# Performance work log

Measured on AMD Instinct MI355X. Metric: run time of the kernel, lower is better.

Reference implementation:

```python
import itertools
import jax, jax.numpy as jnp
import numpy as np

# ---- static config (matches init_kwargs) ----
FRAME_H, FRAME_W = 480, 640
RES = 5               # map_resolution (cm/cell)
Z_RES = 5
MAP_SIZE_CM = 4800 // 2   # after global_downscaling
VR = 100              # vision_range
HFOV = 79.0
DU = 1                # du_scale
CAT_THR, EXP_THR, MAP_THR = 5.0, 1.0, 1.0
NSEM = 16
MAX_H = int(360 / Z_RES)    # 72
MIN_H = int(-80 / Z_RES)    # -16
AGENT_H_CM = 0.88 * 100.0
XC = (FRAME_W - 1.0) / 2.0
ZC = (FRAME_H - 1.0) / 2.0
FOCAL = (FRAME_W / 2.0) / np.tan(np.deg2rad(HFOV / 2.0))
VFOV = np.arctan(FRAME_H / 2.0 / FOCAL)
MIN_VISION = AGENT_H_CM / np.tan(VFOV)
SHIFT_X = VR * RES // 2     # shift_loc[0]; rotation angle is 0 -> identity
DEG = 57.29577951308232


def splat_feat_nd(grid_dims, feat, coords):
    # feat: (B,F,N); coords: (B,3,N) in [-1,1]; trilinear scatter-add splat.
    B, Fc, N = feat.shape
    pos_dim, wts_dim = [], []
    for d in range(3):
        g = grid_dims[d]
        pos = coords[:, d, :] * (g / 2.0) + g / 2.0
        pd, wd = [], []
        for ix in (0, 1):
            p = jnp.floor(pos) + ix
            safe = ((p > 0) & (p < g)).astype(feat.dtype)
            wd.append((1.0 - jnp.abs(pos - p)) * safe)
            pd.append(p * safe)
        pos_dim.append(pd)
        wts_dim.append(wd)
    gflat = jnp.zeros((B, Fc, grid_dims[0] * grid_dims[1] * grid_dims[2]), feat.dtype)
    scatter = jax.vmap(lambda g, i, u: g.at[:, i].add(u))
    for ix_d in itertools.product((0, 1), (0, 1), (0, 1)):
        index = jnp.zeros((B, N), feat.dtype)
        wts = jnp.ones((B, N), feat.dtype)
        for d in range(3):
            index = index * grid_dims[d] + pos_dim[d][ix_d[d]]
            wts = wts * wts_dim[d][ix_d[d]]
        upd = feat * wts[:, None, :]
        gflat = jnp.round(scatter(gflat, index.astype(jnp.int32), upd))  # torch rounds after each pass
    return gflat.reshape(B, Fc, grid_dims[0], grid_dims[1], grid_dims[2])


def affine_grid(theta, H, W):
    # torch F.affine_grid, align_corners=False (default)
    xs = (2.0 * jnp.arange(W) + 1.0) / W - 1.0
    ys = (2.0 * jnp.arange(H) + 1.0) / H - 1.0
    X, Y = jnp.meshgrid(xs, ys, indexing='xy')          # (H,W)
    base = jnp.stack([X, Y, jnp.ones_like(X)], -1)      # (H,W,3)
    return jnp.einsum('bij,hwj->bhwi', theta, base)     # (B,H,W,2)


def grid_sample(img, grid):
    # bilinear, zeros padding, align_corners=True (as in forward)
    B, C, H, W = img.shape
    x = (grid[..., 0] + 1.0) * 0.5 * (W - 1)
    y = (grid[..., 1] + 1.0) * 0.5 * (H - 1)
    x0 = jnp.floor(x)
    y0 = jnp.floor(y)

    def gather(ix, iy):
        valid = ((ix >= 0) & (ix <= W - 1) & (iy >= 0) & (iy <= H - 1)).astype(img.dtype)
        ic = jnp.clip(ix, 0, W - 1).astype(jnp.int32)
        jc = jnp.clip(iy, 0, H - 1).astype(jnp.int32)
        v = jax.vmap(lambda im, jj, ii: im[:, jj, ii])(img, jc, ic)  # (B,C,Ho,Wo)
        return v * valid[:, None]

    wx1 = x - x0
    wx0 = 1.0 - wx1
    wy1 = y - y0
    wy0 = 1.0 - wy1
    return (gather(x0, y0) * (wx0 * wy0)[:, None]
            + gather(x0 + 1, y0) * (wx1 * wy0)[:, None]
            + gather(x0, y0 + 1) * (wx0 * wy1)[:, None]
            + gather(x0 + 1, y0 + 1) * (wx1 * wy1)[:, None])


def reference(obs, pose_obs, maps_last, poses_last, agent_heights):
    bs, c, h, w = obs.shape
    depth = obs[:, 3]
    # ---- point cloud from depth (camera frame) ----
    Y = depth[:, ::DU, ::DU]
    gx = jnp.arange(w, dtype=obs.dtype)[::DU]            # pixel x (width)
    gz = jnp.arange(h - 1, -1, -1, dtype=obs.dtype)[::DU]  # flipped pixel z (height)
    X = (gx[None, None, :] - XC) * Y / FOCAL
    Z = (gz[None, :, None] - ZC) * Y / FOCAL
    Z = Z + agent_heights * 100.0   # camera elevation 0 -> rotation is identity
    X = X + SHIFT_X                 # shift_loc angle pi/2 -> rotation is identity
    # ---- normalize to [-1,1] voxel coords ----
    Xc = ((X / RES) - VR // 2.0) / VR * 2.0
    Yc = ((Y / RES) - VR // 2.0) / VR * 2.0
    Zc = ((Z / Z_RES) - (MAX_H + MIN_H) // 2.0) / (MAX_H - MIN_H) * 2.0
    coords = jnp.stack([Xc, Yc, Zc], axis=1).reshape(bs, 3, -1)   # (B,3,N)
    # ---- per-point features: [occupancy=1, avg-pooled semantics] ----
    hs, ws = h // DU, w // DU
    sem = obs[:, 4:].reshape(bs, c - 4, hs, DU, ws, DU).mean(axis=(3, 5))
    feat = jnp.concatenate([jnp.ones((bs, 1, hs * ws), obs.dtype),
                            sem.reshape(bs, c - 4, hs * ws)], axis=1)
    # ---- splat into voxel grid, then height-axis projections ----
    voxels = splat_feat_nd((VR, VR, MAX_H - MIN_H), feat, coords).swapaxes(2, 3)
    min_z = int(35 / Z_RES - MIN_H)               # 23
    max_z = int((AGENT_H_CM + 1) / Z_RES - MIN_H)  # 33
    floor_z = int(-35 / Z_RES - MIN_H)             # 9
    agent_height_proj = voxels[..., min_z:max_z].sum(-1)
    all_height_proj = voxels.sum(-1)
    mv_std = int(MIN_VISION // Z_RES)
    around_floor = voxels[..., :min_z].sum(-1)
    under_floor = (voxels[..., floor_z:min_z].sum(-1) == 0.0).astype(obs.dtype) * around_floor
    # near-field floor heuristic from last depth row
    depth_row = depth[:, -1, :]
    re_depth = jnp.where(depth_row < 3000.0, depth_row, jnp.asarray(MIN_VISION, obs.dtype))
    count = (re_depth - MIN_VISION - 60.0 > 0).sum(axis=1)
    mask = count > (w / 4.0)
    c1, c2 = (VR - 6) // 2, (VR + 6) // 2
    patch = under_floor[:, 0, mv_std, c1:c2]
    under_floor = under_floor.at[:, 0, mv_std, c1:c2].set(jnp.where(mask[:, None], 1.0, patch))
    fp_map_pred = jnp.clip((agent_height_proj[:, 0:1] + under_floor[:, 0:1]) / MAP_THR, 0.0, 1.0)
    fp_exp_pred = jnp.clip(all_height_proj[:, 0:1] / EXP_THR, 0.0, 1.0)
    # ---- paste into egocentric local map frame ----
    M = MAP_SIZE_CM // RES   # 480
    x1 = M // 2 - VR // 2
    x2 = x1 + VR
    y1 = M // 2
    y2 = y1 + VR
    agent_view = jnp.zeros((bs, c, M, M), obs.dtype)
    agent_view = agent_view.at[:, 0:1, y1:y2, x1:x2].set(fp_map_pred)
    agent_view = agent_view.at[:, 1:2, y1:y2, x1:x2].set(fp_exp_pred)
    agent_view = agent_view.at[:, 4:, y1:y2, x1:x2].set(
        jnp.clip(agent_height_proj[:, 1:] / CAT_THR, 0.0, 1.0))
    # ---- dead-reckoning pose update ----
    th = poses_last[:, 2] / DEG
    ny = poses_last[:, 1] + pose_obs[:, 0] * jnp.sin(th) + pose_obs[:, 1] * jnp.cos(th)
    nx = poses_last[:, 0] + pose_obs[:, 0] * jnp.cos(th) - pose_obs[:, 1] * jnp.sin(th)
    nt = poses_last[:, 2] + pose_obs[:, 2] * DEG
    nt = jnp.fmod(nt - 180.0, 360.0) + 180.0
    nt = jnp.fmod(nt + 180.0, 360.0) - 180.0
    current_poses = jnp.stack([nx, ny, nt], axis=1)
    # ---- spatial transform (rotate then translate) into allocentric map ----
    half = M // 2
    stx = -(nx * 100.0 / RES - half) / half
    sty = -(ny * 100.0 / RES - half) / half
    t = (90.0 - nt) * np.pi / 180.0
    cos_t, sin_t = jnp.cos(t), jnp.sin(t)
    zeros, ones = jnp.zeros_like(cos_t), jnp.ones_like(cos_t)
    theta1 = jnp.stack([jnp.stack([cos_t, -sin_t, zeros], 1),
                        jnp.stack([sin_t, cos_t, zeros], 1)], 1)
    theta2 = jnp.stack([jnp.stack([ones, zeros, stx], 1),
                        jnp.stack([zeros, ones, sty], 1)], 1)
    rotated = grid_sample(agent_view, affine_grid(theta1, M, M))
    translated = grid_sample(rotated, affine_grid(theta2, M, M))
    map_pred = jnp.maximum(maps_last, translated)
    # pose_pred aliases the in-place-updated poses_last in torch == current_poses
    return fp_map_pred, map_pred, current_poses, current_poses


def setup_inputs():
    key = jax.random.key(0)
    k1, k2, k3, k4, k5, k6 = jax.random.split(key, 6)
    bs, c, h, w = 8, 4 + NSEM, FRAME_H, FRAME_W
    obs = jax.random.uniform(k1, (bs, c, h, w), jnp.float32)            # RGB/sem in [0,1]
    depth = jax.random.uniform(k2, (bs, h, w), jnp.float32) * 480.0 + 20.0  # cm
    obs = obs.at[:, 3].set(depth)
    pose_obs = jax.random.normal(k3, (bs, 3), jnp.float32) * jnp.array([0.1, 0.1, 0.05], jnp.float32)
    maps_last = jax.random.uniform(k4, (bs, c, 480, 480), jnp.float32)
    xy = jax.random.uniform(k5, (bs, 2), jnp.float32) * 4.0 + 10.0      # meters, near map center
    ang = jax.random.uniform(k6, (bs, 1), jnp.float32) * 360.0 - 180.0
    poses_last = jnp.concatenate([xy, ang], axis=1)
    agent_heights = jnp.full((bs, 1, 1), 0.88, jnp.float32)
    return {"obs": obs, "pose_obs": pose_obs, "maps_last": maps_last,
            "poses_last": poses_last, "agent_heights": agent_heights}
```

## Files before the change

### kernel.cpp

```cpp
#include <hip/hip_runtime.h>
#include <math.h>

#pragma clang fp contract(off)

#define BS 8
#define CCH 20
#define IMH 480
#define IMW 640
#define HW (IMH*IMW)
#define VRX 100
#define NZ 88
#define NSEMC 16
#define CROP0 124
#define CROPN 232
#define NROTC 18
#define NBINS 880000
#define NBINS2 80000
#define SEMCAP 650000u

__global__ void posemask_kernel(const float* __restrict__ pose_obs,
                                const float* __restrict__ poses_last,
                                const float* __restrict__ obs,
                                float* __restrict__ outp1, float* __restrict__ outp2,
                                float* __restrict__ posebuf, float MINVF) {
#pragma clang fp contract(off)
  int b = blockIdx.x;
  int t = threadIdx.x;
  if (t == 0) {
    const float DEGF = (float)57.29577951308232;
    float th = poses_last[b*3+2] / DEGF;
    float sn = sinf(th), cs = cosf(th);
    float ny = poses_last[b*3+1] + pose_obs[b*3+0]*sn + pose_obs[b*3+1]*cs;
    float nx = poses_last[b*3+0] + pose_obs[b*3+0]*cs - pose_obs[b*3+1]*sn;
    float nt = poses_last[b*3+2] + pose_obs[b*3+2]*DEGF;
    nt = fmodf(nt - 180.0f, 360.0f) + 180.0f;
    nt = fmodf(nt + 180.0f, 360.0f) - 180.0f;
    outp1[b*3+0] = nx; outp1[b*3+1] = ny; outp1[b*3+2] = nt;
    outp2[b*3+0] = nx; outp2[b*3+1] = ny; outp2[b*3+2] = nt;
    float tt = (90.0f - nt) * (float)M_PI / 180.0f;
    float* pb = posebuf + b*8;
    pb[0] = cosf(tt);
    pb[1] = sinf(tt);
    pb[2] = -((nx*100.0f/5.0f - 240.0f)/240.0f);
    pb[3] = -((ny*100.0f/5.0f - 240.0f)/240.0f);
  }
  const float* row = obs + (size_t)b*CCH*HW + 3*(size_t)HW + 479*IMW;
  int cnt = 0;
  for (int col = t; col < IMW; col += 256) {
    float d = row[col];
    float re = (d < 3000.0f) ? d : MINVF;
    float v = re - MINVF;
    v = v - 60.0f;
    if (v > 0.0f) cnt++;
  }
  __shared__ int sh[256];
  sh[t] = cnt;
  __syncthreads();
  for (int s = 128; s > 0; s >>= 1) {
    if (t < s) sh[t] += sh[t + s];
    __syncthreads();
  }
  if (t == 0) posebuf[b*8+4] = (sh[0] > 160) ? 1.0f : 0.0f;
}

__device__ __forceinline__ void transform_pix(int r, int col, float Yd, float ah100,
                                              float FOCALF,
                                              float& pos0, float& pos1, float& pos2) {
#pragma clang fp contract(off)
  float X = ((float)col - 319.5f) * Yd / FOCALF;
  X = X + 250.0f;
  float Z = ((float)(479 - r) - 239.5f) * Yd / FOCALF;
  Z = Z + ah100;
  float Xc = (X/5.0f - 50.0f)/100.0f*2.0f;
  float Yc = (Yd/5.0f - 50.0f)/100.0f*2.0f;
  float Zc = (Z/5.0f - 28.0f)/88.0f*2.0f;
  pos0 = Xc*50.0f + 50.0f;
  pos1 = Yc*50.0f + 50.0f;
  pos2 = Zc*44.0f + 44.0f;
}

__global__ void bin_count_kernel(const float* __restrict__ obs,
                                 const float* __restrict__ agent_h,
                                 unsigned* __restrict__ cnt, unsigned* __restrict__ cnt2,
                                 float FOCALF) {
#pragma clang fp contract(off)
  int tid = blockIdx.x*256 + threadIdx.x;
#pragma unroll
  for (int u = 0; u < 4; u++) {
    int p = tid + u*614400;
    int b = p / HW;
    int pix = p - b*HW;
    int r = pix / IMW, col = pix - r*IMW;
    float Yd = obs[(size_t)b*CCH*HW + 3*(size_t)HW + pix];
    float ah100 = agent_h[b]*100.0f;
    float pos0, pos1, pos2;
    transform_pix(r, col, Yd, ah100, FOCALF, pos0, pos1, pos2);
    float f0 = floorf(pos0), f1 = floorf(pos1), f2 = floorf(pos2);
    if (f0 >= 0.0f && f0 <= 99.0f && f1 >= 0.0f && f1 <= 99.0f &&
        f2 >= 0.0f && f2 <= 87.0f) {
      int xi = (int)f0, yi = (int)f1, zi = (int)f2;
      int cb = (b*100 + yi)*100 + xi;
      atomicAdd(&cnt[cb*11 + (zi >> 3)], 1u);
      if (zi >= 22 && zi <= 32) atomicAdd(&cnt2[cb], 1u);
    }
  }
}

__device__ __forceinline__ void scan1_body(unsigned* cnt_inout,
                                           unsigned* bsum,
                                           int n, int blk, unsigned* sh) {
  int t = threadIdx.x;
  int base = blk*1024 + t*4;
  unsigned v[4];
  unsigned s = 0;
#pragma unroll
  for (int i = 0; i < 4; i++) {
    unsigned c = (base + i < n) ? cnt_inout[base + i] : 0u;
    v[i] = s; s += c;
  }
  sh[t] = s;
  __syncthreads();
  for (int off = 1; off < 256; off <<= 1) {
    unsigned add = (t >= off) ? sh[t - off] : 0u;
    __syncthreads();
    sh[t] += add;
    __syncthreads();
  }
  unsigned texcl = sh[t] - s;
#pragma unroll
  for (int i = 0; i < 4; i++)
    if (base + i < n) cnt_inout[base + i] = texcl + v[i];
  if (t == 255) bsum[blk] = sh[255];
}

__global__ void scan1m_kernel(unsigned* cnt, unsigned* bsum,
                              unsigned* cnt2, unsigned* bsum2) {
  __shared__ unsigned sh[256];
  int blk = blockIdx.x;
  if (blk < 860) scan1_body(cnt, bsum, NBINS, blk, sh);
  else           scan1_body(cnt2, bsum2, NBINS2, blk - 860, sh);
}

__global__ void scan2m_kernel(unsigned* __restrict__ bsum, unsigned* __restrict__ bsum2) {
  __shared__ unsigned sh[1024];
  unsigned* arr = (blockIdx.x == 0) ? bsum : bsum2;
  int nb = (blockIdx.x == 0) ? 860 : 79;
  int t = threadIdx.x;
  unsigned v = (t < nb) ? arr[t] : 0u;
  sh[t] = v;
  __syncthreads();
  for (int off = 1; off < 1024; off <<= 1) {
    unsigned add = (t >= off) ? sh[t - off] : 0u;
    __syncthreads();
    sh[t] += add;
    __syncthreads();
  }
  if (t < nb) arr[t] = sh[t] - v;
}

__global__ void scan3m_kernel(unsigned* __restrict__ offs, const unsigned* __restrict__ bsum,
                              unsigned* __restrict__ offs2, const unsigned* __restrict__ bsum2) {
  int blk = blockIdx.x;
  if (blk < 3438) {
    int i = blk*256 + threadIdx.x;
    if (i >= NBINS) return;
    offs[i] = offs[i] + bsum[i >> 10];
  } else {
    int i = (blk - 3438)*256 + threadIdx.x;
    if (i >= NBINS2) return;
    offs2[i] = offs2[i] + bsum2[i >> 10];
  }
}

__global__ void place_kernel(const float* __restrict__ obs,
                             const float* __restrict__ agent_h,
                             unsigned* __restrict__ offs, unsigned* __restrict__ offs2,
                             float2* __restrict__ recs,
                             float4* __restrict__ sempos, float4* __restrict__ semch,
                             float FOCALF) {
#pragma clang fp contract(off)
  int tid = blockIdx.x*256 + threadIdx.x;
#pragma unroll
  for (int u = 0; u < 2; u++) {
    int p = tid + u*1228800;
    int b = p / HW;
    int pix = p - b*HW;
    int r = pix / IMW, c = pix - r*IMW;
    const float* obsb = obs + (size_t)b*CCH*HW;
    float Yd = obsb[3*(size_t)HW + pix];
    float ah100 = agent_h[b]*100.0f;
    float pos0, pos1, pos2;
    transform_pix(r, c, Yd, ah100, FOCALF, pos0, pos1, pos2);
    float f0 = floorf(pos0), f1 = floorf(pos1), f2 = floorf(pos2);
    if (f0 >= 0.0f && f0 <= 99.0f && f1 >= 0.0f && f1 <= 99.0f &&
        f2 >= 0.0f && f2 <= 87.0f) {
      int xi = (int)f0, yi = (int)f1, zi = (int)f2;
      int cb = (b*100 + yi)*100 + xi;
      unsigned idx = atomicAdd(&offs[cb*11 + (zi >> 3)], 1u);
      recs[idx] = make_float2(__uint_as_float((unsigned)pix), Yd);
      if (zi >= 22 && zi <= 32) {
        unsigned i2 = atomicAdd(&offs2[cb], 1u);
        if (i2 < SEMCAP) {
          sempos[i2] = make_float4(pos0, pos1, pos2, 0.0f);
          float4* cp = semch + (size_t)i2*4;
#pragma unroll
          for (int q = 0; q < 4; q++) {
            cp[q] = make_float4(obsb[(size_t)(4 + q*4 + 0)*HW + pix],
                                obsb[(size_t)(4 + q*4 + 1)*HW + pix],
                                obsb[(size_t)(4 + q*4 + 2)*HW + pix],
                                obsb[(size_t)(4 + q*4 + 3)*HW + pix]);
          }
        }
      }
    }
  }
}

__global__ void __launch_bounds__(256) gatherS_cm_kernel(
    const float2* __restrict__ recs, const unsigned* __restrict__ offs,
    const float* __restrict__ agent_h, float* __restrict__ colbuf, float FOCALF) {
#pragma clang fp contract(off)
  __shared__ float S[256*9];
  __shared__ float red[32][8][4];
  int t = threadIdx.x;
  int k = t & 7, cw = t >> 3;
  int iz = k & 1, ix = (k >> 1) & 1, iy = (k >> 2) & 1;
  int col = blockIdx.x*32 + cw;
  int b = col / 10000;
  int cx = col % 100, cy = (col/100) % 100;
  float ah100 = agent_h[b]*100.0f;
  bool cellvalid = (cx+ix >= 1) && (cx+ix <= 99) && (cy+iy >= 1) && (cy+iy <= 99);
  float fx = (float)ix, fy = (float)iy, fz = (float)iz;
  float* Sl = &S[t*9];
#pragma unroll
  for (int i = 0; i < 8; i++) Sl[i] = 0.0f;
  float pall = 0.f, pahp = 0.f, par = 0.f, pmid = 0.f;
  int colkey = col*11;
  unsigned s = (colkey == 0) ? 0u : offs[colkey - 1];
  for (int oct = 0; oct < 11; oct++) {
    unsigned e = offs[colkey + oct];
    for (unsigned base = s; base < e; base += 8) {
      int nc = (int)min(8u, e - base);
      float p0 = 0.f, p1 = 0.f, p2 = 0.f;
      if (base + (unsigned)k < e) {
        float2 rec = recs[base + k];
        unsigned pix = __float_as_uint(rec.x);
        int rr = pix / IMW, cc = pix - rr*IMW;
        transform_pix(rr, cc, rec.y, ah100, FOCALF, p0, p1, p2);
      }
      for (int c = 0; c < nc; c++) {
        float q0 = __shfl(p0, c, 8);
        float q1 = __shfl(p1, c, 8);
        float q2 = __shfl(p2, c, 8);
        float f0 = floorf(q0), f1 = floorf(q1), f2 = floorf(q2);
        float wx = 1.0f - fabsf(q0 - (f0 + fx));
        float wy = 1.0f - fabsf(q1 - (f1 + fy));
        float wz = 1.0f - fabsf(q2 - (f2 + fz));
        float w = wx*wy;
        w = w*wz;
        int z8 = ((int)f2) & 7;
        Sl[z8] += w;
      }
    }
    s = e;
    int zbase = oct*8;
#pragma unroll
    for (int z8 = 0; z8 < 8; z8++) {
      float a = Sl[z8];
      Sl[z8] = 0.0f;
      int tz = zbase + z8 + iz;
      if (a != 0.0f && tz >= 1 && tz <= 87) {
        float rv = rintf(a);
        pall += rv;
        if (tz < 23) { par += rv; if (tz >= 9) pmid += rv; }
        else if (tz < 33) pahp += rv;
      }
    }
  }
  if (!cellvalid) { pall = 0.f; pahp = 0.f; par = 0.f; pmid = 0.f; }
  red[cw][k][0] = pall;
  red[cw][k][1] = pahp;
  red[cw][k][2] = par;
  red[cw][k][3] = pmid;
  __syncthreads();
  for (int e2 = t; e2 < 512; e2 += 256) {
    int cw2 = e2 >> 4, rem = e2 & 15, c = rem >> 2, p = rem & 3;
    int colw = blockIdx.x*32 + cw2;
    colbuf[colw*16 + rem] = red[cw2][2*c][p] + red[cw2][2*c + 1][p];
  }
}

__global__ void combine_kernel(const float* __restrict__ colbuf,
                               const float* __restrict__ posebuf,
                               float* __restrict__ out0, float* __restrict__ fpexp) {
#pragma clang fp contract(off)
  int tid = blockIdx.x*256 + threadIdx.x;
  if (tid >= 80000) return;
  int b = tid / 10000;
  int yx = tid - b*10000;
  int ty = yx / 100, tx = yx - (yx/100)*100;
  float all = 0.f, ahp = 0.f, ar = 0.f, mid = 0.f;
#pragma unroll
  for (int c = 0; c < 4; c++) {
    int iy = c >> 1, ix = c & 1;
    int cy = ty - iy, cx = tx - ix;
    if (cy < 0 || cx < 0) continue;
    const float* cb = &colbuf[((b*10000 + cy*100 + cx)*4 + c)*4];
    all += cb[0]; ahp += cb[1]; ar += cb[2]; mid += cb[3];
  }
  float u = (mid == 0.0f) ? ar : 0.0f;
  if (ty == 28 && tx >= 47 && tx < 53) {
    if (posebuf[b*8+4] != 0.0f) u = 1.0f;
  }
  float fm = ahp + u;
  out0[tid] = fminf(fmaxf(fm, 0.0f), 1.0f);
  fpexp[tid] = fminf(fmaxf(all, 0.0f), 1.0f);
}

__global__ void __launch_bounds__(128) gatherSem3_kernel(
    const float4* __restrict__ sempos, const float* __restrict__ semch,
    const unsigned* __restrict__ offs2, float* __restrict__ semacc) {
#pragma clang fp contract(off)
  __shared__ float st[128*81];
  int t = threadIdx.x;
  int ch = t & 15;
  int colb = blockIdx.x*8 + (t >> 4);
  int b = colb / 10000;
  int cy = (colb/100) % 100, cx = colb % 100;
  float* S = &st[t*81];
#pragma unroll
  for (int i = 0; i < 80; i++) S[i] = 0.0f;
  unsigned s = (colb == 0) ? 0u : offs2[colb - 1];
  unsigned e = offs2[colb];
  for (unsigned ri = s; ri < e; ri++) {
    float4 pr = sempos[ri];
    float pos0 = pr.x, pos1 = pr.y, pos2 = pr.z;
    float chv = semch[(size_t)ri*16 + ch];
    float f0 = floorf(pos0), f1 = floorf(pos1), f2 = floorf(pos2);
    int zi = (int)f2;
    float wx0 = 1.0f - fabsf(pos0 - f0);
    float wx1 = 1.0f - fabsf(pos0 - (f0 + 1.0f));
    float wy0 = 1.0f - fabsf(pos1 - f1);
    float wy1 = 1.0f - fabsf(pos1 - (f1 + 1.0f));
    float w00 = wx0*wy0;
    float w01 = wx1*wy0;
    float w10 = wx0*wy1;
    float w11 = wx1*wy1;
    float wza = 1.0f - fabsf(pos2 - f2);
    float wzb = 1.0f - fabsf(pos2 - (f2 + 1.0f));
#pragma unroll
    for (int iz = 0; iz < 2; iz++) {
      int tzr = zi + iz - 23;
      if (tzr < 0 || tzr > 9) continue;
      float wz = (iz == 0) ? wza : wzb;
      int base = tzr*8 + iz*4;
      S[base + 0] += chv*(w00*wz);
      S[base + 1] += chv*(w01*wz);
      S[base + 2] += chv*(w10*wz);
      S[base + 3] += chv*(w11*wz);
    }
  }
  float s00 = 0.f, s01 = 0.f, s10 = 0.f, s11 = 0.f;
#pragma unroll
  for (int q = 0; q < 20; q++) {
    s00 += rintf(S[q*4 + 0]);
    s01 += rintf(S[q*4 + 1]);
    s10 += rintf(S[q*4 + 2]);
    s11 += rintf(S[q*4 + 3]);
  }
  float* sa = semacc + ((size_t)b*NSEMC + ch)*10000;
  bool vx0 = (cx >= 1), vx1 = (cx <= 98), vy0 = (cy >= 1), vy1 = (cy <= 98);
  if (vy0 && vx0 && s00 != 0.f) atomicAdd(&sa[cy*100 + cx],           s00);
  if (vy0 && vx1 && s01 != 0.f) atomicAdd(&sa[cy*100 + cx + 1],       s01);
  if (vy1 && vx0 && s10 != 0.f) atomicAdd(&sa[(cy + 1)*100 + cx],     s10);
  if (vy1 && vx1 && s11 != 0.f) atomicAdd(&sa[(cy + 1)*100 + cx + 1], s11);
}

__device__ __forceinline__ float fetch_av(const float* __restrict__ out0,
                                          const float* __restrict__ fpexp,
                                          const float* __restrict__ semacc,
                                          int b, int cidx, float xf, float yf) {
  if (!(xf >= 0.0f && xf <= 479.0f && yf >= 0.0f && yf <= 479.0f)) return 0.0f;
  int xi = (int)xf, yi = (int)yf;
  int wx = xi - 190, wy = yi - 240;
  if (wx < 0 || wx >= 100 || wy < 0 || wy >= 100) return 0.0f;
  int o = b*10000 + wy*100 + wx;
  if (cidx == 0) return out0[o];
  if (cidx == 1) return fpexp[o];
  float v = semacc[(size_t)(b*NSEMC + (cidx-2))*10000 + wy*100 + wx] / 5.0f;
  return fminf(fmaxf(v, 0.0f), 1.0f);
}

__global__ void rotate_kernel(const float* __restrict__ out0, const float* __restrict__ fpexp,
                              const float* __restrict__ semacc,
                              const float* __restrict__ posebuf,
                              float* __restrict__ rot) {
#pragma clang fp contract(off)
  int tid = blockIdx.x*256 + threadIdx.x;
  if (tid >= BS*NROTC*CROPN*CROPN) return;
  int cj = tid % CROPN;
  int t1 = tid / CROPN;
  int ci = t1 % CROPN;
  int t2 = t1 / CROPN;
  int cidx = t2 % NROTC;
  int b = t2 / NROTC;
  int i = ci + CROP0, j = cj + CROP0;
  float X = (2.0f*(float)j + 1.0f)/480.0f - 1.0f;
  float Y = (2.0f*(float)i + 1.0f)/480.0f - 1.0f;
  const float* pb = posebuf + b*8;
  float gx = pb[0]*X - pb[1]*Y;
  float gy = pb[1]*X + pb[0]*Y;
  float x = (gx + 1.0f)*0.5f*479.0f;
  float y = (gy + 1.0f)*0.5f*479.0f;
  float x0 = floorf(x), y0 = floorf(y);
  float wx1 = x - x0, wx0 = 1.0f - wx1;
  float wy1 = y - y0, wy0 = 1.0f - wy1;
  float v00 = fetch_av(out0,fpexp,semacc,b,cidx,x0,       y0);
  float v10 = fetch_av(out0,fpexp,semacc,b,cidx,x0+1.0f,  y0);
  float v01 = fetch_av(out0,fpexp,semacc,b,cidx,x0,       y0+1.0f);
  float v11 = fetch_av(out0,fpexp,semacc,b,cidx,x0+1.0f,  y0+1.0f);
  float val = v00*(wx0*wy0) + v10*(wx1*wy0) + v01*(wx0*wy1) + v11*(wx1*wy1);
  rot[tid] = val;
}

__device__ __forceinline__ float fetch_rot(const float* __restrict__ rot,
                                           int b, int cidx, float xf, float yf) {
  if (!(xf >= 0.0f && xf <= 479.0f && yf >= 0.0f && yf <= 479.0f)) return 0.0f;
  int xi = (int)xf, yi = (int)yf;
  int rx = xi - CROP0, ry = yi - CROP0;
  if (rx < 0 || rx >= CROPN || ry < 0 || ry >= CROPN) return 0.0f;
  return rot[((size_t)(b*NROTC + cidx)*CROPN + ry)*CROPN + rx];
}

__global__ void translate_kernel(const float* __restrict__ maps_last,
                                 const float* __restrict__ rot,
                                 const float* __restrict__ posebuf,
                                 float* __restrict__ out1) {
#pragma clang fp contract(off)
  int tid = blockIdx.x*256 + threadIdx.x;
  if (tid >= 9216000) return;
  int q = tid % 120;
  int t1 = tid / 120;
  int i = t1 % 480;
  int t2 = t1 / 480;
  int c = t2 % CCH;
  int b = t2 / CCH;
  size_t base = (size_t)tid * 4;
  float4 ml = *(const float4*)&maps_last[base];
  if (c == 2 || c == 3) { *(float4*)&out1[base] = ml; return; }
  int cidx = (c < 2) ? c : c - 2;
  const float* pb = posebuf + b*8;
  float Y = (2.0f*(float)i + 1.0f)/480.0f - 1.0f;
  float gy = Y + pb[3];
  float y = (gy + 1.0f)*0.5f*479.0f;
  float y0 = floorf(y);
  float wy1 = y - y0, wy0 = 1.0f - wy1;
  float res[4];
  const float* mlp = (const float*)&ml;
#pragma unroll
  for (int e = 0; e < 4; e++) {
    int j = q*4 + e;
    float X = (2.0f*(float)j + 1.0f)/480.0f - 1.0f;
    float gx = X + pb[2];
    float x = (gx + 1.0f)*0.5f*479.0f;
    float x0 = floorf(x);
    float wx1 = x - x0, wx0 = 1.0f - wx1;
    float v00 = fetch_rot(rot,b,cidx,x0,      y0);
    float v10 = fetch_rot(rot,b,cidx,x0+1.0f, y0);
    float v01 = fetch_rot(rot,b,cidx,x0,      y0+1.0f);
    float v11 = fetch_rot(rot,b,cidx,x0+1.0f, y0+1.0f);
    float val = v00*(wx0*wy0) + v10*(wx1*wy0) + v01*(wx0*wy1) + v11*(wx1*wy1);
    res[e] = fmaxf(mlp[e], val);
  }
  *(float4*)&out1[base] = make_float4(res[0], res[1], res[2], res[3]);
}

extern "C" void kernel_launch(void* const* d_in, const int* in_sizes, int n_in,
                              void* d_out, int out_size, void* d_ws, size_t ws_size,
                              hipStream_t stream) {
  const float* obs        = (const float*)d_in[0];
  const float* pose_obs   = (const float*)d_in[1];
  const float* maps_last  = (const float*)d_in[2];
  const float* poses_last = (const float*)d_in[3];
  const float* agent_h    = (const float*)d_in[4];
  float* out = (float*)d_out;
  float* ws  = (float*)d_ws;

  const size_t WS_NEED = (size_t)64 + 80000ull + 1280000ull
                       + 880000ull + 80000ull + 1024ull + 1024ull
                       + 4915200ull + 2600000ull + 10400000ull + 1280000ull;
  if (ws_size < WS_NEED*sizeof(float)) return;

  double focal_d = 640.0/2.0/tan(79.0/2.0*M_PI/180.0);
  float FOCALF = (float)focal_d;
  double vfov = atan(480.0/2.0/focal_d);
  float MINVF = (float)((0.88*100.0)/tan(vfov));

  float* posebuf = ws;
  float* fpexp   = ws + 64;
  float* semacc  = fpexp + 80000;
  unsigned* cnt   = (unsigned*)(semacc + 1280000);
  unsigned* cnt2  = cnt + 880000;
  unsigned* bsum  = cnt2 + 80000;
  unsigned* bsum2 = bsum + 1024;
  float* bigbuf   = (float*)(bsum2 + 1024);
  float2* recs    = (float2*)bigbuf;
  float4* sempos  = (float4*)(bigbuf + 4915200);
  float4* semch   = (float4*)(bigbuf + 4915200 + 2600000);
  float* colbuf   = bigbuf + 4915200 + 2600000 + 10400000;
  float* rot      = bigbuf;

  float* out0  = out;
  float* out1  = out + 80000;
  float* outp1 = out1 + (size_t)BS*CCH*480*480;
  float* outp2 = outp1 + 24;

  hipMemsetAsync(semacc, 0, 1280000ull*sizeof(float), stream);
  hipMemsetAsync(cnt, 0, ((size_t)880000 + 80000ull)*sizeof(unsigned), stream);

  posemask_kernel<<<BS, 256, 0, stream>>>(pose_obs, poses_last, obs,
                                          outp1, outp2, posebuf, MINVF);
  bin_count_kernel<<<2400, 256, 0, stream>>>(obs, agent_h, cnt, cnt2, FOCALF);
  scan1m_kernel<<<939, 256, 0, stream>>>(cnt, bsum, cnt2, bsum2);
  scan2m_kernel<<<2, 1024, 0, stream>>>(bsum, bsum2);
  scan3m_kernel<<<3751, 256, 0, stream>>>(cnt, bsum, cnt2, bsum2);

  place_kernel<<<4800, 256, 0, stream>>>(obs, agent_h, cnt, cnt2,
                                         recs, sempos, semch, FOCALF);
  gatherS_cm_kernel<<<2500, 256, 0, stream>>>(recs, cnt, agent_h, colbuf, FOCALF);
  combine_kernel<<<313, 256, 0, stream>>>(colbuf, posebuf, out0, fpexp);
  gatherSem3_kernel<<<10000, 128, 0, stream>>>(sempos, (const float*)semch, cnt2, semacc);

  rotate_kernel<<<30276, 256, 0, stream>>>(out0, fpexp, semacc, posebuf, rot);
  translate_kernel<<<36000, 256, 0, stream>>>(maps_last, rot, posebuf, out1);
}
```

Baseline: 677.8 us.

## Merge small kernels into neighbors and batch atomics in place kernel

Folds the pose/mask computation into extra blocks of the bin-count launch, and the combine step into extra blocks of the semantic gather launch, removing two kernel launches and their serialization gaps. The place kernel now handles four pixels per thread with half the blocks. It first computes all keys, then issues the atomics back-to-back, then writes, so atomic latencies overlap. This trades some register pressure and launch occupancy for fewer launches and more memory-level parallelism.

```diff
diff --git a/kernel.cpp b/kernel.cpp
--- a/kernel.cpp
+++ b/kernel.cpp
@@ -18,51 +18,6 @@
 #define NBINS2 80000
 #define SEMCAP 650000u
 
-__global__ void posemask_kernel(const float* __restrict__ pose_obs,
-                                const float* __restrict__ poses_last,
-                                const float* __restrict__ obs,
-                                float* __restrict__ outp1, float* __restrict__ outp2,
-                                float* __restrict__ posebuf, float MINVF) {
-#pragma clang fp contract(off)
-  int b = blockIdx.x;
-  int t = threadIdx.x;
-  if (t == 0) {
-    const float DEGF = (float)57.29577951308232;
-    float th = poses_last[b*3+2] / DEGF;
-    float sn = sinf(th), cs = cosf(th);
-    float ny = poses_last[b*3+1] + pose_obs[b*3+0]*sn + pose_obs[b*3+1]*cs;
-    float nx = poses_last[b*3+0] + pose_obs[b*3+0]*cs - pose_obs[b*3+1]*sn;
-    float nt = poses_last[b*3+2] + pose_obs[b*3+2]*DEGF;
-    nt = fmodf(nt - 180.0f, 360.0f) + 180.0f;
-    nt = fmodf(nt + 180.0f, 360.0f) - 180.0f;
-    outp1[b*3+0] = nx; outp1[b*3+1] = ny; outp1[b*3+2] = nt;
-    outp2[b*3+0] = nx; outp2[b*3+1] = ny; outp2[b*3+2] = nt;
-    float tt = (90.0f - nt) * (float)M_PI / 180.0f;
-    float* pb = posebuf + b*8;
-    pb[0] = cosf(tt);
-    pb[1] = sinf(tt);
-    pb[2] = -((nx*100.0f/5.0f - 240.0f)/240.0f);
-    pb[3] = -((ny*100.0f/5.0f - 240.0f)/240.0f);
-  }
-  const float* row = obs + (size_t)b*CCH*HW + 3*(size_t)HW + 479*IMW;
-  int cnt = 0;
-  for (int col = t; col < IMW; col += 256) {
-    float d = row[col];
-    float re = (d < 3000.0f) ? d : MINVF;
-    float v = re - MINVF;
-    v = v - 60.0f;
-    if (v > 0.0f) cnt++;
-  }
-  __shared__ int sh[256];
-  sh[t] = cnt;
-  __syncthreads();
-  for (int s = 128; s > 0; s >>= 1) {
-    if (t < s) sh[t] += sh[t + s];
-    __syncthreads();
-  }
-  if (t == 0) posebuf[b*8+4] = (sh[0] > 160) ? 1.0f : 0.0f;
-}
-
 __device__ __forceinline__ void transform_pix(int r, int col, float Yd, float ah100,
                                               float FOCALF,
                                               float& pos0, float& pos1, float& pos2) {
@@ -82,9 +37,54 @@
 __global__ void bin_count_kernel(const float* __restrict__ obs,
                                  const float* __restrict__ agent_h,
                                  unsigned* __restrict__ cnt, unsigned* __restrict__ cnt2,
-                                 float FOCALF) {
-#pragma clang fp contract(off)
-  int tid = blockIdx.x*256 + threadIdx.x;
+                                 const float* __restrict__ pose_obs,
+                                 const float* __restrict__ poses_last,
+                                 float* __restrict__ outp1, float* __restrict__ outp2,
+                                 float* __restrict__ posebuf,
+                                 float FOCALF, float MINVF) {
+#pragma clang fp contract(off)
+  int blk = blockIdx.x;
+  if (blk >= 2400) {
+    int b = blk - 2400;
+    int t = threadIdx.x;
+    if (t == 0) {
+      const float DEGF = (float)57.29577951308232;
+      float th = poses_last[b*3+2] / DEGF;
+      float sn = sinf(th), cs = cosf(th);
+      float ny = poses_last[b*3+1] + pose_obs[b*3+0]*sn + pose_obs[b*3+1]*cs;
+      float nx = poses_last[b*3+0] + pose_obs[b*3+0]*cs - pose_obs[b*3+1]*sn;
+      float nt = poses_last[b*3+2] + pose_obs[b*3+2]*DEGF;
+      nt = fmodf(nt - 180.0f, 360.0f) + 180.0f;
+      nt = fmodf(nt + 180.0f, 360.0f) - 180.0f;
+      outp1[b*3+0] = nx; outp1[b*3+1] = ny; outp1[b*3+2] = nt;
+      outp2[b*3+0] = nx; outp2[b*3+1] = ny; outp2[b*3+2] = nt;
+      float tt = (90.0f - nt) * (float)M_PI / 180.0f;
+      float* pb = posebuf + b*8;
+      pb[0] = cosf(tt);
+      pb[1] = sinf(tt);
+      pb[2] = -((nx*100.0f/5.0f - 240.0f)/240.0f);
+      pb[3] = -((ny*100.0f/5.0f - 240.0f)/240.0f);
+    }
+    const float* row = obs + (size_t)b*CCH*HW + 3*(size_t)HW + 479*IMW;
+    int c2 = 0;
+    for (int col = t; col < IMW; col += 256) {
+      float d = row[col];
+      float re = (d < 3000.0f) ? d : MINVF;
+      float v = re - MINVF;
+      v = v - 60.0f;
+      if (v > 0.0f) c2++;
+    }
+    __shared__ int sh[256];
+    sh[t] = c2;
+    __syncthreads();
+    for (int s = 128; s > 0; s >>= 1) {
+      if (t < s) sh[t] += sh[t + s];
+      __syncthreads();
+    }
+    if (t == 0) posebuf[b*8+4] = (sh[0] > 160) ? 1.0f : 0.0f;
+    return;
+  }
+  int tid = blk*256 + threadIdx.x;
 #pragma unroll
   for (int u = 0; u < 4; u++) {
     int p = tid + u*614400;
@@ -180,9 +180,14 @@
                              float FOCALF) {
 #pragma clang fp contract(off)
   int tid = blockIdx.x*256 + threadIdx.x;
-#pragma unroll
-  for (int u = 0; u < 2; u++) {
-    int p = tid + u*1228800;
+  int   keyv[4];
+  float2 payv[4];
+  int   semk[4];
+  float4 spv[4];
+  int   pixv[4];
+#pragma unroll
+  for (int u = 0; u < 4; u++) {
+    int p = tid + u*614400;
     int b = p / HW;
     int pix = p - b*HW;
     int r = pix / IMW, c = pix - r*IMW;
@@ -192,25 +197,46 @@
     float pos0, pos1, pos2;
     transform_pix(r, c, Yd, ah100, FOCALF, pos0, pos1, pos2);
     float f0 = floorf(pos0), f1 = floorf(pos1), f2 = floorf(pos2);
+    keyv[u] = -1; semk[u] = -1;
+    pixv[u] = pix;
+    payv[u] = make_float2(__uint_as_float((unsigned)pix), Yd);
     if (f0 >= 0.0f && f0 <= 99.0f && f1 >= 0.0f && f1 <= 99.0f &&
         f2 >= 0.0f && f2 <= 87.0f) {
       int xi = (int)f0, yi = (int)f1, zi = (int)f2;
       int cb = (b*100 + yi)*100 + xi;
-      unsigned idx = atomicAdd(&offs[cb*11 + (zi >> 3)], 1u);
-      recs[idx] = make_float2(__uint_as_float((unsigned)pix), Yd);
+      keyv[u] = cb*11 + (zi >> 3);
       if (zi >= 22 && zi <= 32) {
-        unsigned i2 = atomicAdd(&offs2[cb], 1u);
-        if (i2 < SEMCAP) {
-          sempos[i2] = make_float4(pos0, pos1, pos2, 0.0f);
-          float4* cp = semch + (size_t)i2*4;
-#pragma unroll
-          for (int q = 0; q < 4; q++) {
-            cp[q] = make_float4(obsb[(size_t)(4 + q*4 + 0)*HW + pix],
-                                obsb[(size_t)(4 + q*4 + 1)*HW + pix],
-                                obsb[(size_t)(4 + q*4 + 2)*HW + pix],
-                                obsb[(size_t)(4 + q*4 + 3)*HW + pix]);
-          }
-        }
+        semk[u] = cb;
+        spv[u] = make_float4(pos0, pos1, pos2, 0.0f);
+      }
+    }
+  }
+  unsigned idxv[4];
+#pragma unroll
+  for (int u = 0; u < 4; u++)
+    if (keyv[u] >= 0) idxv[u] = atomicAdd(&offs[keyv[u]], 1u);
+#pragma unroll
+  for (int u = 0; u < 4; u++)
+    if (keyv[u] >= 0) recs[idxv[u]] = payv[u];
+  unsigned sidv[4];
+#pragma unroll
+  for (int u = 0; u < 4; u++)
+    if (semk[u] >= 0) sidv[u] = atomicAdd(&offs2[semk[u]], 1u);
+#pragma unroll
+  for (int u = 0; u < 4; u++) {
+    if (semk[u] >= 0 && sidv[u] < SEMCAP) {
+      int p = tid + u*614400;
+      int b = p / HW;
+      const float* obsb = obs + (size_t)b*CCH*HW;
+      int pix = pixv[u];
+      sempos[sidv[u]] = spv[u];
+      float4* cp = semch + (size_t)sidv[u]*4;
+#pragma unroll
+      for (int q = 0; q < 4; q++) {
+        cp[q] = make_float4(obsb[(size_t)(4 + q*4 + 0)*HW + pix],
+                            obsb[(size_t)(4 + q*4 + 1)*HW + pix],
+                            obsb[(size_t)(4 + q*4 + 2)*HW + pix],
+                            obsb[(size_t)(4 + q*4 + 3)*HW + pix]);
       }
     }
   }
@@ -290,39 +316,38 @@
   }
 }
 
-__global__ void combine_kernel(const float* __restrict__ colbuf,
-                               const float* __restrict__ posebuf,
-                               float* __restrict__ out0, float* __restrict__ fpexp) {
-#pragma clang fp contract(off)
-  int tid = blockIdx.x*256 + threadIdx.x;
-  if (tid >= 80000) return;
-  int b = tid / 10000;
-  int yx = tid - b*10000;
-  int ty = yx / 100, tx = yx - (yx/100)*100;
-  float all = 0.f, ahp = 0.f, ar = 0.f, mid = 0.f;
-#pragma unroll
-  for (int c = 0; c < 4; c++) {
-    int iy = c >> 1, ix = c & 1;
-    int cy = ty - iy, cx = tx - ix;
-    if (cy < 0 || cx < 0) continue;
-    const float* cb = &colbuf[((b*10000 + cy*100 + cx)*4 + c)*4];
-    all += cb[0]; ahp += cb[1]; ar += cb[2]; mid += cb[3];
-  }
-  float u = (mid == 0.0f) ? ar : 0.0f;
-  if (ty == 28 && tx >= 47 && tx < 53) {
-    if (posebuf[b*8+4] != 0.0f) u = 1.0f;
-  }
-  float fm = ahp + u;
-  out0[tid] = fminf(fmaxf(fm, 0.0f), 1.0f);
-  fpexp[tid] = fminf(fmaxf(all, 0.0f), 1.0f);
-}
-
 __global__ void __launch_bounds__(128) gatherSem3_kernel(
     const float4* __restrict__ sempos, const float* __restrict__ semch,
-    const unsigned* __restrict__ offs2, float* __restrict__ semacc) {
+    const unsigned* __restrict__ offs2, float* __restrict__ semacc,
+    const float* __restrict__ colbuf, const float* __restrict__ posebuf,
+    float* __restrict__ out0, float* __restrict__ fpexp) {
 #pragma clang fp contract(off)
   __shared__ float st[128*81];
   int t = threadIdx.x;
+  if (blockIdx.x >= 10000) {
+    int tid = (blockIdx.x - 10000)*128 + t;
+    if (tid >= 80000) return;
+    int b = tid / 10000;
+    int yx = tid - b*10000;
+    int ty = yx / 100, tx = yx - (yx/100)*100;
+    float all = 0.f, ahp = 0.f, ar = 0.f, mid = 0.f;
+#pragma unroll
+    for (int c = 0; c < 4; c++) {
+      int iy = c >> 1, ix = c & 1;
+      int cy = ty - iy, cx = tx - ix;
+      if (cy < 0 || cx < 0) continue;
+      const float* cb = &colbuf[((b*10000 + cy*100 + cx)*4 + c)*4];
+      all += cb[0]; ahp += cb[1]; ar += cb[2]; mid += cb[3];
+    }
+    float u = (mid == 0.0f) ? ar : 0.0f;
+    if (ty == 28 && tx >= 47 && tx < 53) {
+      if (posebuf[b*8+4] != 0.0f) u = 1.0f;
+    }
+    float fm = ahp + u;
+    out0[tid] = fminf(fmaxf(fm, 0.0f), 1.0f);
+    fpexp[tid] = fminf(fmaxf(all, 0.0f), 1.0f);
+    return;
+  }
   int ch = t & 15;
   int colb = blockIdx.x*8 + (t >> 4);
   int b = colb / 10000;
@@ -518,18 +543,19 @@
   hipMemsetAsync(semacc, 0, 1280000ull*sizeof(float), stream);
   hipMemsetAsync(cnt, 0, ((size_t)880000 + 80000ull)*sizeof(unsigned), stream);
 
-  posemask_kernel<<<BS, 256, 0, stream>>>(pose_obs, poses_last, obs,
-                                          outp1, outp2, posebuf, MINVF);
-  bin_count_kernel<<<2400, 256, 0, stream>>>(obs, agent_h, cnt, cnt2, FOCALF);
+  bin_count_kernel<<<2408, 256, 0, stream>>>(obs, agent_h, cnt, cnt2,
+                                             pose_obs, poses_last,
+                                             outp1, outp2, posebuf,
+                                             FOCALF, MINVF);
   scan1m_kernel<<<939, 256, 0, stream>>>(cnt, bsum, cnt2, bsum2);
   scan2m_kernel<<<2, 1024, 0, stream>>>(bsum, bsum2);
   scan3m_kernel<<<3751, 256, 0, stream>>>(cnt, bsum, cnt2, bsum2);
 
-  place_kernel<<<4800, 256, 0, stream>>>(obs, agent_h, cnt, cnt2,
+  place_kernel<<<2400, 256, 0, stream>>>(obs, agent_h, cnt, cnt2,
                                          recs, sempos, semch, FOCALF);
   gatherS_cm_kernel<<<2500, 256, 0, stream>>>(recs, cnt, agent_h, colbuf, FOCALF);
-  combine_kernel<<<313, 256, 0, stream>>>(colbuf, posebuf, out0, fpexp);
-  gatherSem3_kernel<<<10000, 128, 0, stream>>>(sempos, (const float*)semch, cnt2, semacc);
+  gatherSem3_kernel<<<10625, 128, 0, stream>>>(sempos, (const float*)semch, cnt2, semacc,
+                                               colbuf, posebuf, out0, fpexp);
 
   rotate_kernel<<<30276, 256, 0, stream>>>(out0, fpexp, semacc, posebuf, rot);
   translate_kernel<<<36000, 256, 0, stream>>>(maps_last, rot, posebuf, out1);
```

Measured after the change: 751.7 us. +10.9%, slower.
